# Optimization experiments

Measured on AMD Instinct MI355X. Metric: run time of the kernel, lower is better.

The kernel has to match this reference:

```python
import jax, jax.numpy as jnp
import numpy as np

NUM_HEADS = 16
EPS = 1e-6  # torch LayerNorm default is 1e-5; module uses nn.LayerNorm default
LN_EPS = 1e-5


def layer_norm(x, w, b, eps=LN_EPS):
    # normalize over last dim (head_dim), matching infer_layer_norm
    mu = jnp.mean(x, axis=-1, keepdims=True)
    xc = x - mu
    var = jnp.mean(xc * xc, axis=-1, keepdims=True)
    return xc / jnp.sqrt(var + eps) * w + b


def setup_inputs() -> dict:
    key = jax.random.key(0)
    ks = jax.random.split(key, 4)
    B, N, C = 2, 4096, 1024
    H = NUM_HEADS
    D = C // H
    x = jax.random.normal(ks[0], (B, N, C), dtype=jnp.float32)
    qkv_w = jax.random.normal(ks[1], (3 * C, C), dtype=jnp.float32) * (C ** -0.5)
    qkv_b = jax.random.normal(ks[2], (3 * C,), dtype=jnp.float32) * 0.02
    q_norm_w = jnp.ones((D,), dtype=jnp.float32)
    q_norm_b = jnp.zeros((D,), dtype=jnp.float32)
    k_norm_w = jnp.ones((D,), dtype=jnp.float32)
    k_norm_b = jnp.zeros((D,), dtype=jnp.float32)
    proj_w = jax.random.normal(ks[3], (C, C), dtype=jnp.float32) * (C ** -0.5)
    proj_b = jnp.zeros((C,), dtype=jnp.float32)
    return {"x": x, "qkv_w": qkv_w, "qkv_b": qkv_b,
            "q_norm_w": q_norm_w, "q_norm_b": q_norm_b,
            "k_norm_w": k_norm_w, "k_norm_b": k_norm_b,
            "proj_w": proj_w, "proj_b": proj_b}


def reference(x, qkv_w, qkv_b, q_norm_w, q_norm_b, k_norm_w, k_norm_b, proj_w, proj_b):
    B, N, C = x.shape
    H = NUM_HEADS
    D = C // H
    scale = D ** -0.5
    # QKV projection: torch Linear uses y = x @ W^T + b
    qkv = x @ qkv_w.T + qkv_b                      # [B,N,3C]
    qkv = qkv.reshape(B, N, 3, H, D).transpose(2, 0, 3, 1, 4)  # [3,B,H,N,D]
    q, k, v = qkv[0], qkv[1], qkv[2]
    # per-head qk layernorm
    q = layer_norm(q, q_norm_w, q_norm_b)
    k = layer_norm(k, k_norm_w, k_norm_b)
    # scaled dot product attention
    attn = jnp.einsum('bhqd,bhkd->bhqk', q * scale, k)
    attn = jax.nn.softmax(attn, axis=-1)
    out = jnp.einsum('bhqk,bhkd->bhqd', attn, v)   # [B,H,N,D]
    out = out.transpose(0, 2, 1, 3).reshape(B, N, C)
    return out @ proj_w.T + proj_b
```

## Files before the change

### kernel.cpp

```cpp
#include <hip/hip_runtime.h>
#include <hip/hip_bf16.h>

#define NB 2
#define NN 4096
#define NC 1024
#define NH 16
#define ND 64
#define NM (NB*NN)
#define NK 1024
#define J_QKV 3072
#define QSCALE 0.18033688011112042f

typedef unsigned short u16;
typedef unsigned int   u32;
typedef __attribute__((ext_vector_type(8)))  __bf16 bf16x8;
typedef __attribute__((ext_vector_type(4)))  float  f32x4;
typedef __attribute__((ext_vector_type(16))) float  f32x16;

__device__ __forceinline__ u16 f2bf(float f) {
    unsigned int i = __builtin_bit_cast(unsigned int, f);
    unsigned int lsb = (i >> 16) & 1u;
    i += 0x7fffu + lsb;
    return (u16)(i >> 16);
}
__device__ __forceinline__ float fast_exp2(float x) {
#if __has_builtin(__builtin_amdgcn_exp2f)
    return __builtin_amdgcn_exp2f(x);
#else
    return exp2f(x);
#endif
}
__device__ __forceinline__ u32 pkbf(float a, float b) {
    u32 r;
    asm("v_cvt_pk_bf16_f32 %0, %1, %2" : "=v"(r) : "v"(a), "v"(b));
    return r;
}
typedef struct { u32 x, y; } u32pair;
__device__ __forceinline__ u32pair swap32(u32 a, u32 b) {
#if __has_builtin(__builtin_amdgcn_permlane32_swap)
    auto r = __builtin_amdgcn_permlane32_swap((int)a, (int)b, false, false);
    u32pair o; o.x = (u32)r[0]; o.y = (u32)r[1]; return o;
#else
    const bool hi = (threadIdx.x & 32) != 0;
    u32 as = (u32)__shfl_xor((int)a, 32);
    u32 bs = (u32)__shfl_xor((int)b, 32);
    u32pair o; o.x = hi ? bs : a; o.y = hi ? b : as; return o;
#endif
}

__device__ __forceinline__ void glds16(const u16* g, u16* l) {
    __builtin_amdgcn_global_load_lds(
        (const __attribute__((address_space(1))) u32*)g,
        (__attribute__((address_space(3))) u32*)l, 16, 0, 0);
}

__global__ __launch_bounds__(256) void cvt3(
    const float* __restrict__ a, u16* __restrict__ oa,
    const float* __restrict__ b, u16* __restrict__ ob,
    const float* __restrict__ c, u16* __restrict__ oc)
{
    const int blk = blockIdx.x;
    const float* src; u16* dst; size_t off;
    if (blk < 4096)      { src = a; dst = oa; off = (size_t)blk * 2048; }
    else if (blk < 5632) { src = b; dst = ob; off = (size_t)(blk - 4096) * 2048; }
    else                 { src = c; dst = oc; off = (size_t)(blk - 5632) * 2048; }
    const size_t i = off + (size_t)threadIdx.x * 8;
    const float4 va = *(const float4*)(src + i);
    const float4 vb = *(const float4*)(src + i + 4);
    union { u16 h[8]; uint4 v; } u;
    u.h[0] = f2bf(va.x); u.h[1] = f2bf(va.y); u.h[2] = f2bf(va.z); u.h[3] = f2bf(va.w);
    u.h[4] = f2bf(vb.x); u.h[5] = f2bf(vb.y); u.h[6] = f2bf(vb.z); u.h[7] = f2bf(vb.w);
    *(uint4*)(dst + i) = u.v;
}

template<int MODE, int NJB>
__global__ __launch_bounds__(256, 3) void gemm_nt(
    const u16* __restrict__ A, const u16* __restrict__ W,
    const float* __restrict__ bias,
    const float* __restrict__ qw, const float* __restrict__ qb,
    const float* __restrict__ kw, const float* __restrict__ kb,
    void* __restrict__ outv)
{
    __shared__ __align__(16) u16 sm[4][128][32];
    const int t = threadIdx.x;
    const int w = t >> 6, lane = t & 63;
    const int nb   = blockIdx.x;
    const int cpx  = gridDim.x >> 3;
    const int nb2  = (nb & 7) * cpx + (nb >> 3);
    const int chunk = nb2 / cpx;
    const int c     = nb2 - chunk * cpx;
    const int jb  = (c >> 3) * 128;
    const int m0  = (chunk * 8 + (c & 7)) * 128;
    const int wr = (w >> 1) * 64, wc = (w & 1) * 64;
    const int srow = t >> 2, skc = (t & 3) * 8;
    const u16* ap0 = A + (size_t)(m0 + srow) * NK + skc;
    const u16* ap1 = ap0 + (size_t)64 * NK;
    const u16* wp0 = W + (size_t)(jb + srow) * NK + skc;
    const u16* wp1 = wp0 + (size_t)64 * NK;
    u16* asl0 = &sm[0][srow][skc];    u16* asl1 = &sm[0][srow + 64][skc];
    u16* ash0 = &sm[1][srow][skc];    u16* ash1 = &sm[1][srow + 64][skc];
    u16* bsl0 = &sm[2][srow][skc];    u16* bsl1 = &sm[2][srow + 64][skc];
    u16* bsh0 = &sm[3][srow][skc];    u16* bsh1 = &sm[3][srow + 64][skc];
    const int fm = lane & 15, fk = 8 * (lane >> 4);
    f32x4 acc[4][4];
    #pragma unroll
    for (int i = 0; i < 4; ++i)
        #pragma unroll
        for (int j = 0; j < 4; ++j) acc[i][j] = (f32x4){0.f, 0.f, 0.f, 0.f};

    for (int kt = 0; kt < NK / 64; ++kt) {
        const int ko = kt * 64;
        glds16(ap0 + ko, asl0);
        glds16(ap1 + ko, asl1);
        glds16(ap0 + ko + 32, ash0);
        glds16(ap1 + ko + 32, ash1);
        glds16(wp0 + ko, bsl0);
        glds16(wp1 + ko, bsl1);
        glds16(wp0 + ko + 32, bsh0);
        glds16(wp1 + ko + 32, bsh1);
        __syncthreads();
        {
            bf16x8 af[4], bfr[4];
            #pragma unroll
            for (int i = 0; i < 4; ++i) af[i]  = *(const bf16x8*)&sm[0][wr + 16 * i + fm][fk];
            #pragma unroll
            for (int j = 0; j < 4; ++j) bfr[j] = *(const bf16x8*)&sm[2][wc + 16 * j + fm][fk];
            #pragma unroll
            for (int i = 0; i < 4; ++i)
                #pragma unroll
                for (int j = 0; j < 4; ++j)
                    acc[i][j] = __builtin_amdgcn_mfma_f32_16x16x32_bf16(af[i], bfr[j], acc[i][j], 0, 0, 0);
        }
        {
            bf16x8 af[4], bfr[4];
            #pragma unroll
            for (int i = 0; i < 4; ++i) af[i]  = *(const bf16x8*)&sm[1][wr + 16 * i + fm][fk];
            #pragma unroll
            for (int j = 0; j < 4; ++j) bfr[j] = *(const bf16x8*)&sm[3][wc + 16 * j + fm][fk];
            #pragma unroll
            for (int i = 0; i < 4; ++i)
                #pragma unroll
                for (int j = 0; j < 4; ++j)
                    acc[i][j] = __builtin_amdgcn_mfma_f32_16x16x32_bf16(af[i], bfr[j], acc[i][j], 0, 0, 0);
        }
        __syncthreads();
    }
    const int c16 = lane & 15;
    float bv[4];
    #pragma unroll
    for (int j = 0; j < 4; ++j) bv[j] = bias[jb + wc + 16 * j + c16];
    #pragma unroll
    for (int i = 0; i < 4; ++i)
        #pragma unroll
        for (int j = 0; j < 4; ++j)
            #pragma unroll
            for (int r = 0; r < 4; ++r) acc[i][j][r] += bv[j];
    if (MODE == 0) {
        const int s = jb >> 10;
        if (s < 2) {
            const float* lw = s ? kw : qw;
            const float* lb = s ? kb : qb;
            float lwv[4], lbv[4];
            #pragma unroll
            for (int j = 0; j < 4; ++j) {
                lwv[j] = lw[16 * j + c16]; lbv[j] = lb[16 * j + c16];
            }
            #pragma unroll
            for (int i = 0; i < 4; ++i)
                #pragma unroll
                for (int r = 0; r < 4; ++r) {
                    float sum = acc[i][0][r] + acc[i][1][r] + acc[i][2][r] + acc[i][3][r];
                    #pragma unroll
                    for (int off = 1; off < 16; off <<= 1) sum += __shfl_xor(sum, off);
                    const float mu = sum * (1.0f / 64.0f);
                    float v2 = 0.f;
                    #pragma unroll
                    for (int j = 0; j < 4; ++j) { const float dd = acc[i][j][r] - mu; v2 += dd * dd; }
                    #pragma unroll
                    for (int off = 1; off < 16; off <<= 1) v2 += __shfl_xor(v2, off);
                    const float rstd = rsqrtf(v2 * (1.0f / 64.0f) + 1e-5f);
                    #pragma unroll
                    for (int j = 0; j < 4; ++j) {
                        float y = (acc[i][j][r] - mu) * rstd * lwv[j] + lbv[j];
                        if (s == 0) y *= QSCALE;
                        acc[i][j][r] = y;
                    }
                }
        }
        u16 (*bounce)[128] = (u16 (*)[128])sm;
        const int r0 = 4 * (lane >> 4);
        #pragma unroll
        for (int i = 0; i < 4; ++i)
            #pragma unroll
            for (int r = 0; r < 4; ++r)
                #pragma unroll
                for (int j = 0; j < 4; ++j)
                    bounce[wr + 16 * i + r0 + r][wc + 16 * j + c16] = f2bf(acc[i][j][r]);
        __syncthreads();
        u16* out = (u16*)outv;
        const int l8 = lane >> 3, k8 = lane & 7;
        #pragma unroll
        for (int ch = 0; ch < 2; ++ch) {
            const int col0 = jb + ch * 64;
            const int ss = col0 >> 10, hh = (col0 >> 6) & 15;
            #pragma unroll
            for (int g = 0; g < 4; ++g) {
                const int rr = 32 * w + 8 * g + l8;
                const int row = m0 + rr;
                const int b_ = row >> 12, n = row & 4095;
                const uint4 v = *(const uint4*)&bounce[rr][ch * 64 + k8 * 8];
                *(uint4*)&out[((((size_t)ss * NB + b_) * NH + hh) * NN + n) * ND + k8 * 8] = v;
            }
        }
    } else {
        float* out = (float*)outv;
        const int r0 = 4 * (lane >> 4);
        #pragma unroll
        for (int i = 0; i < 4; ++i)
            #pragma unroll
            for (int r = 0; r < 4; ++r) {
                const int row = m0 + wr + 16 * i + r0 + r;
                #pragma unroll
                for (int j = 0; j < 4; ++j)
                    out[(size_t)row * NC + jb + wc + 16 * j + c16] = acc[i][j][r];
            }
    }
}

__global__ __launch_bounds__(256, 2) void attn_mfma(
    const u16* __restrict__ qkv, u16* __restrict__ aout)
{
    __shared__ __align__(16) u16 Ks[2][64][72];
    __shared__ __align__(16) u16 Vt[2][64][72];
    const int bid  = blockIdx.x;
    const int qblk = bid & 15;
    const int bh   = bid >> 4;
    const int b = bh >> 4, hh = bh & 15;
    const size_t plane = (size_t)NB * NH * NN * ND;
    const size_t base  = ((size_t)(b * NH + hh)) * NN * ND;
    const u16* qp = qkv + base;
    const u16* kp = qkv + plane + base;
    const u16* vp = qkv + 2 * plane + base;
    const int t = threadIdx.x, w = t >> 6, lane = t & 63;
    const int half = lane >> 5, m32 = lane & 31;
    const int q0 = qblk * 256 + 64 * w;

    bf16x8 qf[2][4];
    #pragma unroll
    for (int s = 0; s < 2; ++s) {
        const u16* qrow = qp + (size_t)(q0 + 32 * s + m32) * ND + 8 * half;
        #pragma unroll
        for (int kt = 0; kt < 4; ++kt) qf[s][kt] = *(const bf16x8*)(qrow + 16 * kt);
    }
    f32x16 O[2][2], L[2], z;
    #pragma unroll
    for (int r = 0; r < 16; ++r) {
        O[0][0][r] = 0.f; O[0][1][r] = 0.f;
        O[1][0][r] = 0.f; O[1][1][r] = 0.f;
        L[0][r] = 0.f;    L[1][r] = 0.f;    z[r] = 0.f;
    }
    union { u32 wd[4]; bf16x8 f; } ONE1;
    #pragma unroll
    for (int i = 0; i < 4; ++i) ONE1.wd[i] = 0x3F803F80u;

    const int dgK = 16 * w;
    const int kp2 = t & 31, dgV = (t >> 5) * 8;
    const u16* ksrc = kp + (size_t)lane * ND + dgK;
    const u16* vsrc = vp + (size_t)(2 * kp2) * ND + dgV;

    uint4 kr0, kr1, vre, vro;
    kr0 = *(const uint4*)(ksrc);
    kr1 = *(const uint4*)(ksrc + 8);
    vre = *(const uint4*)(vsrc);
    vro = *(const uint4*)(vsrc + ND);
    {
        *(uint4*)&Ks[0][lane][dgK]     = kr0;
        *(uint4*)&Ks[0][lane][dgK + 8] = kr1;
        const u32* ew = (const u32*)&vre;
        const u32* ow = (const u32*)&vro;
        #pragma unroll
        for (int d = 0; d < 4; ++d) {
            u32 lo = __builtin_amdgcn_perm(ow[d], ew[d], 0x05040100u);
            u32 hi = __builtin_amdgcn_perm(ow[d], ew[d], 0x07060302u);
            *(u32*)&Vt[0][dgV + 2 * d][2 * kp2]     = lo;
            *(u32*)&Vt[0][dgV + 2 * d + 1][2 * kp2] = hi;
        }
    }
    __syncthreads();

    union W8 { u32 wd[4]; bf16x8 f; };

    for (int kb = 0; kb < NN / 64; ++kb) {
        const int cur = kb & 1, nxt = cur ^ 1;
        const bool more = (kb + 1) < (NN / 64);
        if (more) {
            const u16* ks2 = ksrc + (size_t)(kb + 1) * 64 * ND;
            kr0 = *(const uint4*)ks2;
            kr1 = *(const uint4*)(ks2 + 8);
            const u16* vs2 = vsrc + (size_t)(kb + 1) * 64 * ND;
            vre = *(const uint4*)vs2;
            vro = *(const uint4*)(vs2 + ND);
        }
        f32x16 sT0[2], sT1[2];
        __builtin_amdgcn_s_setprio(1);
        {
            bf16x8 k0 = *(const bf16x8*)&Ks[cur][m32][8 * half];
            bf16x8 k1 = *(const bf16x8*)&Ks[cur][32 + m32][8 * half];
            sT0[0] = __builtin_amdgcn_mfma_f32_32x32x16_bf16(k0, qf[0][0], z, 0, 0, 0);
            sT0[1] = __builtin_amdgcn_mfma_f32_32x32x16_bf16(k1, qf[0][0], z, 0, 0, 0);
        }
        #pragma unroll
        for (int kt = 1; kt < 4; ++kt) {
            bf16x8 k0 = *(const bf16x8*)&Ks[cur][m32][16 * kt + 8 * half];
            bf16x8 k1 = *(const bf16x8*)&Ks[cur][32 + m32][16 * kt + 8 * half];
            sT0[0] = __builtin_amdgcn_mfma_f32_32x32x16_bf16(k0, qf[0][kt], sT0[0], 0, 0, 0);
            sT0[1] = __builtin_amdgcn_mfma_f32_32x32x16_bf16(k1, qf[0][kt], sT0[1], 0, 0, 0);
        }
        {
            bf16x8 k0 = *(const bf16x8*)&Ks[cur][m32][8 * half];
            bf16x8 k1 = *(const bf16x8*)&Ks[cur][32 + m32][8 * half];
            sT1[0] = __builtin_amdgcn_mfma_f32_32x32x16_bf16(k0, qf[1][0], z, 0, 0, 0);
            sT1[1] = __builtin_amdgcn_mfma_f32_32x32x16_bf16(k1, qf[1][0], z, 0, 0, 0);
        }
        #pragma unroll
        for (int kt = 1; kt < 4; ++kt) {
            bf16x8 k0 = *(const bf16x8*)&Ks[cur][m32][16 * kt + 8 * half];
            bf16x8 k1 = *(const bf16x8*)&Ks[cur][32 + m32][16 * kt + 8 * half];
            sT1[0] = __builtin_amdgcn_mfma_f32_32x32x16_bf16(k0, qf[1][kt], sT1[0], 0, 0, 0);
            sT1[1] = __builtin_amdgcn_mfma_f32_32x32x16_bf16(k1, qf[1][kt], sT1[1], 0, 0, 0);
        }
        __builtin_amdgcn_s_setprio(0);
        W8 pa0[4], pa1[4];
        #pragma unroll
        for (int kh = 0; kh < 2; ++kh) {
            float p[16];
            #pragma unroll
            for (int r = 0; r < 16; ++r) p[r] = fast_exp2(sT0[kh][r]);
            u32 c[4][2];
            #pragma unroll
            for (int g = 0; g < 4; ++g) {
                c[g][0] = pkbf(p[4 * g + 0], p[4 * g + 1]);
                c[g][1] = pkbf(p[4 * g + 2], p[4 * g + 3]);
            }
            #pragma unroll
            for (int par = 0; par < 2; ++par) {
                u32pair wA = swap32(c[2 * par][0], c[2 * par + 1][0]);
                u32pair wB = swap32(c[2 * par][1], c[2 * par + 1][1]);
                const int kt = 2 * kh + par;
                pa0[kt].wd[0] = wA.x;
                pa0[kt].wd[1] = wB.x;
                pa0[kt].wd[2] = wA.y;
                pa0[kt].wd[3] = wB.y;
            }
        }
        __builtin_amdgcn_s_setprio(1);
        #pragma unroll
        for (int kt = 0; kt < 4; ++kt) {
            bf16x8 v0 = *(const bf16x8*)&Vt[cur][m32][16 * kt + 8 * half];
            bf16x8 v1 = *(const bf16x8*)&Vt[cur][32 + m32][16 * kt + 8 * half];
            O[0][0] = __builtin_amdgcn_mfma_f32_32x32x16_bf16(pa0[kt].f, v0, O[0][0], 0, 0, 0);
            O[0][1] = __builtin_amdgcn_mfma_f32_32x32x16_bf16(pa0[kt].f, v1, O[0][1], 0, 0, 0);
            L[0]    = __builtin_amdgcn_mfma_f32_32x32x16_bf16(pa0[kt].f, ONE1.f, L[0], 0, 0, 0);
        }
        __builtin_amdgcn_s_setprio(0);
        #pragma unroll
        for (int kh = 0; kh < 2; ++kh) {
            float p[16];
            #pragma unroll
            for (int r = 0; r < 16; ++r) p[r] = fast_exp2(sT1[kh][r]);
            u32 c[4][2];
            #pragma unroll
            for (int g = 0; g < 4; ++g) {
                c[g][0] = pkbf(p[4 * g + 0], p[4 * g + 1]);
                c[g][1] = pkbf(p[4 * g + 2], p[4 * g + 3]);
            }
            #pragma unroll
            for (int par = 0; par < 2; ++par) {
                u32pair wA = swap32(c[2 * par][0], c[2 * par + 1][0]);
                u32pair wB = swap32(c[2 * par][1], c[2 * par + 1][1]);
                const int kt = 2 * kh + par;
                pa1[kt].wd[0] = wA.x;
                pa1[kt].wd[1] = wB.x;
                pa1[kt].wd[2] = wA.y;
                pa1[kt].wd[3] = wB.y;
            }
        }
        __builtin_amdgcn_s_setprio(1);
        #pragma unroll
        for (int kt = 0; kt < 4; ++kt) {
            bf16x8 v0 = *(const bf16x8*)&Vt[cur][m32][16 * kt + 8 * half];
            bf16x8 v1 = *(const bf16x8*)&Vt[cur][32 + m32][16 * kt + 8 * half];
            O[1][0] = __builtin_amdgcn_mfma_f32_32x32x16_bf16(pa1[kt].f, v0, O[1][0], 0, 0, 0);
            O[1][1] = __builtin_amdgcn_mfma_f32_32x32x16_bf16(pa1[kt].f, v1, O[1][1], 0, 0, 0);
            L[1]    = __builtin_amdgcn_mfma_f32_32x32x16_bf16(pa1[kt].f, ONE1.f, L[1], 0, 0, 0);
        }
        __builtin_amdgcn_s_setprio(0);
        if (more) {
            *(uint4*)&Ks[nxt][lane][dgK]     = kr0;
            *(uint4*)&Ks[nxt][lane][dgK + 8] = kr1;
            const u32* ew = (const u32*)&vre;
            const u32* ow = (const u32*)&vro;
            #pragma unroll
            for (int d = 0; d < 4; ++d) {
                u32 lo = __builtin_amdgcn_perm(ow[d], ew[d], 0x05040100u);
                u32 hi = __builtin_amdgcn_perm(ow[d], ew[d], 0x07060302u);
                *(u32*)&Vt[nxt][dgV + 2 * d][2 * kp2]     = lo;
                *(u32*)&Vt[nxt][dgV + 2 * d + 1][2 * kp2] = hi;
            }
            __syncthreads();
        }
    }
    #pragma unroll
    for (int s = 0; s < 2; ++s) {
        #pragma unroll
        for (int r = 0; r < 16; ++r) {
            const int qq = (r & 3) + 8 * (r >> 2) + 4 * half;
            const float inv = 1.0f / L[s][r];
            const int row = q0 + 32 * s + qq;
            u16* dst = aout + ((size_t)(b * NN + row)) * NC + hh * 64;
            dst[m32]      = f2bf(O[s][0][r] * inv);
            dst[32 + m32] = f2bf(O[s][1][r] * inv);
        }
    }
}

extern "C" void kernel_launch(void* const* d_in, const int* in_sizes, int n_in,
                              void* d_out, int out_size, void* d_ws, size_t ws_size,
                              hipStream_t stream) {
    const float* x     = (const float*)d_in[0];
    const float* qkv_w = (const float*)d_in[1];
    const float* qkv_b = (const float*)d_in[2];
    const float* q_nw  = (const float*)d_in[3];
    const float* q_nb  = (const float*)d_in[4];
    const float* k_nw  = (const float*)d_in[5];
    const float* k_nb  = (const float*)d_in[6];
    const float* p_w   = (const float*)d_in[7];
    const float* p_b   = (const float*)d_in[8];
    float* out = (float*)d_out;
    u16* qkv    = (u16*)d_ws;
    u16* x_bf   = qkv + (size_t)3 * NB * NH * NN * ND;
    u16* attn_o = x_bf;
    u16* w_bf   = x_bf + (size_t)NM * NC;
    u16* pw_bf  = w_bf + (size_t)J_QKV * NK;

    cvt3<<<6144, 256, 0, stream>>>(x, x_bf, qkv_w, w_bf, p_w, pw_bf);

    gemm_nt<0, J_QKV / 128><<<(J_QKV / 128) * (NM / 128), 256, 0, stream>>>(
        x_bf, w_bf, qkv_b, q_nw, q_nb, k_nw, k_nb, qkv);
    attn_mfma<<<NB * NH * (NN / 256), 256, 0, stream>>>(qkv, attn_o);
    gemm_nt<1, NC / 128><<<(NC / 128) * (NM / 128), 256, 0, stream>>>(
        attn_o, pw_bf, p_b, q_nw, q_nb, k_nw, k_nb, out);
}
```

Before: 327.8 us.

## Double-buffer GEMM LDS tiles with K=32 stages and async prefetch

Restructures the GEMM main loop to split K into 32-wide stages held in two LDS buffers. The global-to-LDS loads for stage kt+2 are issued right after computing stage kt, with explicit vmcnt waits and barriers. The aim is to overlap global memory latency with MFMA work instead of waiting on a full load each iteration. The cost is twice as many loop iterations and barriers per K, and correctness now depends on hand-written waitcnt and barrier sequencing.

```diff
diff --git a/kernel.cpp b/kernel.cpp
--- a/kernel.cpp
+++ b/kernel.cpp
@@ -81,7 +81,7 @@
     const float* __restrict__ kw, const float* __restrict__ kb,
     void* __restrict__ outv)
 {
-    __shared__ __align__(16) u16 sm[4][128][32];
+    __shared__ __align__(16) u16 sm[2][2][128][32];
     const int t = threadIdx.x;
     const int w = t >> 6, lane = t & 63;
     const int nb   = blockIdx.x;
@@ -97,10 +97,6 @@
     const u16* ap1 = ap0 + (size_t)64 * NK;
     const u16* wp0 = W + (size_t)(jb + srow) * NK + skc;
     const u16* wp1 = wp0 + (size_t)64 * NK;
-    u16* asl0 = &sm[0][srow][skc];    u16* asl1 = &sm[0][srow + 64][skc];
-    u16* ash0 = &sm[1][srow][skc];    u16* ash1 = &sm[1][srow + 64][skc];
-    u16* bsl0 = &sm[2][srow][skc];    u16* bsl1 = &sm[2][srow + 64][skc];
-    u16* bsh0 = &sm[3][srow][skc];    u16* bsh1 = &sm[3][srow + 64][skc];
     const int fm = lane & 15, fk = 8 * (lane >> 4);
     f32x4 acc[4][4];
     #pragma unroll
@@ -108,43 +104,45 @@
         #pragma unroll
         for (int j = 0; j < 4; ++j) acc[i][j] = (f32x4){0.f, 0.f, 0.f, 0.f};
 
-    for (int kt = 0; kt < NK / 64; ++kt) {
-        const int ko = kt * 64;
-        glds16(ap0 + ko, asl0);
-        glds16(ap1 + ko, asl1);
-        glds16(ap0 + ko + 32, ash0);
-        glds16(ap1 + ko + 32, ash1);
-        glds16(wp0 + ko, bsl0);
-        glds16(wp1 + ko, bsl1);
-        glds16(wp0 + ko + 32, bsh0);
-        glds16(wp1 + ko + 32, bsh1);
-        __syncthreads();
+#define STAGE(ktile, d) do {                                  \
+        const int ko_ = (ktile) * 32;                         \
+        glds16(ap0 + ko_, &sm[d][0][srow][skc]);              \
+        glds16(ap1 + ko_, &sm[d][0][srow + 64][skc]);         \
+        glds16(wp0 + ko_, &sm[d][1][srow][skc]);              \
+        glds16(wp1 + ko_, &sm[d][1][srow + 64][skc]);         \
+    } while (0)
+
+    STAGE(0, 0);
+    STAGE(1, 1);
+    asm volatile("s_waitcnt vmcnt(4)" ::: "memory");
+    asm volatile("s_barrier" ::: "memory");
+
+    for (int kt = 0; kt < NK / 32; ++kt) {
+        const int cur = kt & 1;
         {
             bf16x8 af[4], bfr[4];
             #pragma unroll
-            for (int i = 0; i < 4; ++i) af[i]  = *(const bf16x8*)&sm[0][wr + 16 * i + fm][fk];
-            #pragma unroll
-            for (int j = 0; j < 4; ++j) bfr[j] = *(const bf16x8*)&sm[2][wc + 16 * j + fm][fk];
+            for (int i = 0; i < 4; ++i) af[i]  = *(const bf16x8*)&sm[cur][0][wr + 16 * i + fm][fk];
+            #pragma unroll
+            for (int j = 0; j < 4; ++j) bfr[j] = *(const bf16x8*)&sm[cur][1][wc + 16 * j + fm][fk];
             #pragma unroll
             for (int i = 0; i < 4; ++i)
                 #pragma unroll
                 for (int j = 0; j < 4; ++j)
                     acc[i][j] = __builtin_amdgcn_mfma_f32_16x16x32_bf16(af[i], bfr[j], acc[i][j], 0, 0, 0);
         }
-        {
-            bf16x8 af[4], bfr[4];
-            #pragma unroll
-            for (int i = 0; i < 4; ++i) af[i]  = *(const bf16x8*)&sm[1][wr + 16 * i + fm][fk];
-            #pragma unroll
-            for (int j = 0; j < 4; ++j) bfr[j] = *(const bf16x8*)&sm[3][wc + 16 * j + fm][fk];
-            #pragma unroll
-            for (int i = 0; i < 4; ++i)
-                #pragma unroll
-                for (int j = 0; j < 4; ++j)
-                    acc[i][j] = __builtin_amdgcn_mfma_f32_16x16x32_bf16(af[i], bfr[j], acc[i][j], 0, 0, 0);
-        }
-        __syncthreads();
-    }
+        asm volatile("s_waitcnt lgkmcnt(0)" ::: "memory");
+        asm volatile("s_barrier" ::: "memory");
+        if (kt + 2 < NK / 32) {
+            STAGE(kt + 2, cur);
+            asm volatile("s_waitcnt vmcnt(4)" ::: "memory");
+        } else {
+            asm volatile("s_waitcnt vmcnt(0)" ::: "memory");
+        }
+        asm volatile("s_barrier" ::: "memory");
+    }
+#undef STAGE
+
     const int c16 = lane & 15;
     float bv[4];
     #pragma unroll
```

Result: slower. 344.1 us (+5.0%).
